# Optimization experiments

Hardware: AMD Instinct MI355X
Metric: run time of the kernel (lower is better)

## Reference

```python
import jax, jax.numpy as jnp
import numpy as np

B, S, HID = 1, 4096, 1024
NH, HD = 16, 64            # heads, per-head dim
BS = 256                    # block size
PB = 256                    # position buckets (= max_relative_positions)
EPS = 1e-7


def make_log_bucket_position(rel, num_buckets, max_position):
    sign = jnp.sign(rel)
    max_exact = num_buckets // 2
    in_exact = (rel < max_exact) & (rel > -max_exact)
    abs_pos = jnp.where(in_exact, max_exact - 1, jnp.abs(rel))
    x = jnp.log((max_position - 1) / max_exact)
    xx = jnp.log(abs_pos / max_exact) / x
    log_pos = jnp.ceil(xx * (max_exact - 1)) + max_exact
    return jnp.where(abs_pos <= max_exact, rel, (log_pos * sign).astype(jnp.int32)).astype(jnp.int32)


def split_into_blocks(x, block_size, axis):
    # [..., S, ...] -> [..., S//bs, bs, ...]; S assumed divisible by bs
    shp = x.shape
    new = shp[:axis] + (shp[axis] // block_size, block_size) + shp[axis + 1:]
    return x.reshape(new)


def concat_3_blocks(x, block_axis, seq_axis, pad_value=0):
    # pad one zero block on each side of the block axis, then concat
    # [prev, cur, next] along the within-block seq axis.
    pad = [(0, 0)] * x.ndim
    pad[block_axis] = (1, 1)
    xp = jnp.pad(x, pad, constant_values=pad_value)
    nb = x.shape[block_axis]
    slices = [jax.lax.dynamic_slice_in_dim(xp, i, nb, block_axis) for i in range(3)]
    return jnp.concatenate(slices, axis=seq_axis)


def layer_norm(x, scale, bias):
    mu = jnp.mean(x, axis=-1, keepdims=True)
    var = jnp.mean(jnp.square(x - mu), axis=-1, keepdims=True)
    return (x - mu) * jax.lax.rsqrt(var + EPS) * scale + bias


def setup_inputs() -> dict:
    key = jax.random.key(0)
    ks = jax.random.split(key, 8)
    d = {
        'hidden_states': jax.random.normal(ks[0], (B, S, HID), jnp.float32) * 0.02,
        'rel_pos_embeddings': jax.random.normal(ks[1], (S, HID), jnp.float32) * 0.02,
        'Wq': jax.random.normal(ks[2], (HID, HID), jnp.float32) * 0.01,
        'bq': jnp.zeros((HID,), jnp.float32),
        'Wk': jax.random.normal(ks[3], (HID, HID), jnp.float32) * 0.01,
        'bk': jnp.zeros((HID,), jnp.float32),
        'Wv': jax.random.normal(ks[4], (HID, HID), jnp.float32) * 0.01,
        'bv': jnp.zeros((HID,), jnp.float32),
        'Wo': jax.random.normal(ks[5], (HID, HID), jnp.float32) * 0.01,
        'bo': jnp.zeros((HID,), jnp.float32),
        'ln_scale': jnp.ones((HID,), jnp.float32),
        'ln_bias': jnp.zeros((HID,), jnp.float32),
    }
    return d


def reference(hidden_states, rel_pos_embeddings, Wq, bq, Wk, bk, Wv, bv, Wo, bo, ln_scale, ln_bias):
    b, s, hid = hidden_states.shape

    def heads(x):
        return x.reshape(x.shape[:-1] + (NH, HD))

    # content projections -> [B, nb, bs, h, d]
    q = split_into_blocks(heads(hidden_states @ Wq + bq), BS, axis=1)
    k = split_into_blocks(heads(hidden_states @ Wk + bk), BS, axis=1)
    v = split_into_blocks(heads(hidden_states @ Wv + bv), BS, axis=1)
    k3 = concat_3_blocks(k, block_axis=1, seq_axis=2)   # [B, nb, 3bs, h, d]
    v3 = concat_3_blocks(v, block_axis=1, seq_axis=2)

    c2c = jnp.einsum('bnqhd,bnkhd->bnhqk', q, k3)

    # position projections, stacked over batch (size-1 batch dim broadcasts in einsum)
    pos_q = split_into_blocks(heads(rel_pos_embeddings @ Wq + bq)[None], BS, axis=1)  # [1, nb, bs, h, d]
    pos_k = split_into_blocks(heads(rel_pos_embeddings @ Wk + bk)[None], BS, axis=1)
    pos_k3 = concat_3_blocks(pos_k, block_axis=1, seq_axis=2)                          # [1, nb, 3bs, h, d]

    rel = jnp.arange(BS, dtype=jnp.int32)[:, None] - jnp.arange(3 * BS, dtype=jnp.int32)[None, :]
    rel = make_log_bucket_position(rel, PB, PB)
    idx = jnp.clip(rel + PB, 0, 2 * PB - 1)            # [bs, 3bs]

    c2p = jnp.einsum('bnqhd,bnkhd->bnhqk', q, pos_k3)  # [B, nb, h, bs, 3bs]
    # faithful to the source: axis-less jnp.take gathers from the FLATTENED
    # score tensor -> [bs, 3bs] bias broadcast over (batch, block, head)
    c2p_bias = jnp.take(c2p, idx)

    p2c = jnp.einsum('bnqhd,bnkhd->bnhqk', pos_q, k3)
    p2c_bias = jnp.take(p2c, idx)

    scale = jnp.sqrt(jnp.asarray(HD * 3, hidden_states.dtype))
    attn = (c2c + c2p_bias + p2c_bias) / scale
    probs = jax.nn.softmax(attn, axis=-1)

    ctx = jnp.einsum('bnhqk,bnkhd->bnqhd', probs, v3)  # [B, nb, bs, h, d]
    ctx = ctx.reshape(b, s, hid)
    out = ctx @ Wo + bo
    return layer_norm(out + hidden_states, ln_scale, ln_bias)
```

## Files before the change

### kernel.cpp

```cpp
#include <hip/hip_runtime.h>
#include <stdint.h>

typedef unsigned short u16;
typedef __bf16 bf16_t;
typedef bf16_t v8bf __attribute__((ext_vector_type(8)));
typedef float v4f __attribute__((ext_vector_type(4)));

#define SEQ   4096
#define HIDN  1024
#define NHEAD 16
#define HDIM  64
#define BLK   256
#define NBLK  16

#define GLOAD_LDS16(g, l) __builtin_amdgcn_global_load_lds( \
  (const __attribute__((address_space(1))) unsigned*)(g), \
  (__attribute__((address_space(3))) unsigned*)(l), 16, 0, 0)

__device__ __forceinline__ u16 f2bf(float f){
  union { float f; unsigned u; } v; v.f = f;
  unsigned r = (v.u + 0x7fffu + ((v.u >> 16) & 1u)) >> 16;
  return (u16)r;
}
__device__ __forceinline__ float bf2f(u16 h){
  union { unsigned u; float f; } v; v.u = ((unsigned)h) << 16;
  return v.f;
}

__global__ __launch_bounds__(256) void k_prep(const float* __restrict__ hidden, u16* __restrict__ hb,
    const float* __restrict__ Wq, const float* __restrict__ Wk,
    const float* __restrict__ Wv, const float* __restrict__ Wo, u16* __restrict__ Wt,
    const float* __restrict__ bq, const float* __restrict__ bk, const float* __restrict__ bv,
    float* __restrict__ bcat,
    const float* __restrict__ rpe, float* __restrict__ posk, float* __restrict__ posq0)
{
  __shared__ float t[32][33];
  __shared__ float red[4][64];
  int b = blockIdx.x, tid = threadIdx.x;
  if (b < 4096){
    int w = b >> 10, tile = b & 1023;
    int k0 = (tile & 31) * 32, n0 = (tile >> 5) * 32;
    const float* W = (w == 0) ? Wq : (w == 1) ? Wk : (w == 2) ? Wv : Wo;
    u16* outp = Wt + (size_t)w * 1024 * 1024;
    int x = tid & 31, y = tid >> 5;
    #pragma unroll
    for (int yy = 0; yy < 32; yy += 8) t[y + yy][x] = W[(size_t)(k0 + y + yy) * 1024 + n0 + x];
    __syncthreads();
    #pragma unroll
    for (int yy = 0; yy < 32; yy += 8) outp[(size_t)(n0 + y + yy) * 1024 + k0 + x] = f2bf(t[x][y + yy]);
  } else if (b < 4608){
    int base = (b - 4096) * 8192;
    #pragma unroll
    for (int j = 0; j < 8; j++){
      int i = base + j * 1024 + tid * 4;
      float4 f = *(const float4*)&hidden[i];
      unsigned u0 = (unsigned)f2bf(f.x) | ((unsigned)f2bf(f.y) << 16);
      unsigned u1 = (unsigned)f2bf(f.z) | ((unsigned)f2bf(f.w) << 16);
      uint2 p; p.x = u0; p.y = u1;
      *(uint2*)&hb[i] = p;
    }
  } else if (b == 4608){
    #pragma unroll
    for (int j = 0; j < 12; j++){
      int i = j * 256 + tid;
      const float* src = i < 1024 ? bq : (i < 2048 ? bk : bv);
      bcat[i] = src[i & 1023];
    }
  } else {
    int pb = b - 4609;
    int d = tid & 63, part = tid >> 6;
    const float* W  = (pb < 256) ? Wk : Wq;
    const float* rv = (pb < 256) ? &rpe[(size_t)pb * 1024] : rpe;
    float s = 0.f;
    for (int k = part * 256; k < part * 256 + 256; k++) s += rv[k] * W[(size_t)k * 1024 + d];
    red[part][d] = s;
    __syncthreads();
    if (part == 0){
      s = red[0][d] + red[1][d] + red[2][d] + red[3][d];
      if (pb < 256) posk[pb * 64 + d] = s + bk[d];
      else          posq0[d] = s + bq[d];
    }
  }
}

__global__ __launch_bounds__(256) void k_gemm_qkv(const u16* __restrict__ A, const u16* __restrict__ Bt,
                                                  const float* __restrict__ bias,
                                                  u16* __restrict__ qk, u16* __restrict__ Vt)
{
  __shared__ alignas(16) u16 As[128 * 32];
  __shared__ alignas(16) u16 Bs[128 * 32];
  int tid = threadIdx.x, lane = tid & 63, wid = tid >> 6;
  int wr = wid >> 1, wc = wid & 1;
  int m0 = blockIdx.y * 128, n0 = blockIdx.x * 128;
  const int K = 1024;

  v4f acc[4][4];
  #pragma unroll
  for (int m = 0; m < 4; m++)
    #pragma unroll
    for (int n = 0; n < 4; n++) acc[m][n] = (v4f){0.f, 0.f, 0.f, 0.f};

  int r = lane & 15, g = lane >> 4;
  int ob0 = wid * 2048;

  for (int kt = 0; kt < K; kt += 32){
    #pragma unroll
    for (int t = 0; t < 2; ++t){
      int ob = ob0 + t * 1024;
      int o  = ob + lane * 16;
      int row = o >> 6, col = (o & 63) >> 1;
      GLOAD_LDS16(&A [(size_t)(m0 + row) * K + kt + col], As + (ob >> 1));
      GLOAD_LDS16(&Bt[(size_t)(n0 + row) * K + kt + col], Bs + (ob >> 1));
    }
    __syncthreads();
    v8bf a[4], bb[4];
    #pragma unroll
    for (int m = 0; m < 4; m++) a[m] = *(const v8bf*)&As[(wr * 64 + m * 16 + r) * 32 + g * 8];
    #pragma unroll
    for (int n = 0; n < 4; n++) bb[n] = *(const v8bf*)&Bs[(wc * 64 + n * 16 + r) * 32 + g * 8];
    #pragma unroll
    for (int m = 0; m < 4; m++)
      #pragma unroll
      for (int n = 0; n < 4; n++)
        acc[m][n] = __builtin_amdgcn_mfma_f32_16x16x32_bf16(a[m], bb[n], acc[m][n], 0, 0, 0);
    __syncthreads();
  }

  #pragma unroll
  for (int m = 0; m < 4; m++)
    #pragma unroll
    for (int n = 0; n < 4; n++){
      int col = n0 + wc * 64 + n * 16 + r;
      float bv = bias[col];
      #pragma unroll
      for (int i = 0; i < 4; i++){
        int row = m0 + wr * 64 + m * 16 + g * 4 + i;
        u16 h = f2bf(acc[m][n][i] + bv);
        if (col < 2048) qk[(size_t)row * 2048 + col] = h;
        else            Vt[(size_t)(col - 2048) * 4096 + row] = h;
      }
    }
}

__global__ __launch_bounds__(256) void k_gemm_out(const u16* __restrict__ A, const u16* __restrict__ Bt,
                                                  const float* __restrict__ bias,
                                                  const float* __restrict__ resid, float* __restrict__ Cout)
{
  __shared__ alignas(16) u16 As[128 * 32];
  __shared__ alignas(16) u16 Bs[128 * 32];
  int tid = threadIdx.x, lane = tid & 63, wid = tid >> 6;
  int wr = wid >> 1, wc = wid & 1;
  int m0 = blockIdx.y * 128, n0 = blockIdx.x * 128;
  const int K = 1024;

  v4f acc[4][4];
  #pragma unroll
  for (int m = 0; m < 4; m++)
    #pragma unroll
    for (int n = 0; n < 4; n++) acc[m][n] = (v4f){0.f, 0.f, 0.f, 0.f};

  int r = lane & 15, g = lane >> 4;
  int ob0 = wid * 2048;

  for (int kt = 0; kt < K; kt += 32){
    #pragma unroll
    for (int t = 0; t < 2; ++t){
      int ob = ob0 + t * 1024;
      int o  = ob + lane * 16;
      int row = o >> 6, col = (o & 63) >> 1;
      GLOAD_LDS16(&A [(size_t)(m0 + row) * K + kt + col], As + (ob >> 1));
      GLOAD_LDS16(&Bt[(size_t)(n0 + row) * K + kt + col], Bs + (ob >> 1));
    }
    __syncthreads();
    v8bf a[4], bb[4];
    #pragma unroll
    for (int m = 0; m < 4; m++) a[m] = *(const v8bf*)&As[(wr * 64 + m * 16 + r) * 32 + g * 8];
    #pragma unroll
    for (int n = 0; n < 4; n++) bb[n] = *(const v8bf*)&Bs[(wc * 64 + n * 16 + r) * 32 + g * 8];
    #pragma unroll
    for (int m = 0; m < 4; m++)
      #pragma unroll
      for (int n = 0; n < 4; n++)
        acc[m][n] = __builtin_amdgcn_mfma_f32_16x16x32_bf16(a[m], bb[n], acc[m][n], 0, 0, 0);
    __syncthreads();
  }

  #pragma unroll
  for (int m = 0; m < 4; m++)
    #pragma unroll
    for (int n = 0; n < 4; n++){
      int col = n0 + wc * 64 + n * 16 + r;
      float bv = bias[col];
      #pragma unroll
      for (int i = 0; i < 4; i++){
        int row = m0 + wr * 64 + m * 16 + g * 4 + i;
        Cout[(size_t)row * 1024 + col] = acc[m][n][i] + bv + resid[(size_t)row * 1024 + col];
      }
    }
}

__global__ __launch_bounds__(256) void k_bias(const u16* __restrict__ qk,
                                              const float* __restrict__ posk, const float* __restrict__ posq0,
                                              float* __restrict__ biasd)
{
  __shared__ float brow[512];
  int tid = threadIdx.x;
  brow[tid] = 0.f;
  {
    int u = tid;
    float c2p = 0.f, p2c = 0.f;
    for (int d = 0; d < 64; d++){
      c2p += bf2f(qk[d]) * posk[u * 64 + d];
      p2c += posq0[d] * bf2f(qk[(size_t)u * 2048 + 1024 + d]);
    }
    brow[256 + u] = c2p + p2c;
  }
  __syncthreads();
  #pragma unroll
  for (int j = 0; j < 4; j++){
    int t = tid + j * 256;
    int rel = t - 767;
    int bucket;
    bool in_exact = (rel < 128) && (rel > -128);
    int abs_pos = in_exact ? 127 : (rel < 0 ? -rel : rel);
    if (abs_pos <= 128) bucket = rel;
    else {
      float xx = logf((float)abs_pos * (1.0f / 128.0f)) / logf(255.0f / 128.0f);
      float lp = ceilf(xx * 127.0f) + 128.0f;
      int sgn = (rel > 0) ? 1 : ((rel < 0) ? -1 : 0);
      bucket = (int)lp * sgn;
    }
    int idx = bucket + 256;
    idx = idx < 0 ? 0 : (idx > 511 ? 511 : idx);
    biasd[t] = brow[idx];
  }
}

__global__ __launch_bounds__(256) void k_attn(const u16* __restrict__ qk, const u16* __restrict__ Vt,
                                              const float* __restrict__ biasd, u16* __restrict__ ctxg)
{
  __shared__ alignas(16) u16 Qs[32 * 72];
  __shared__ alignas(16) u16 KVs[128 * 72];
  __shared__ alignas(16) u16 Ss[32 * 776];
  __shared__ float invsum[32];
  __shared__ float bias_s[1024];

  int b = blockIdx.x;
  int qt = b & 7, h = (b >> 3) & 15, n = b >> 7;
  int tid = threadIdx.x, lane = tid & 63, wid = tid >> 6;
  int q0 = n * 256 + qt * 32;
  int qb0 = qt * 32;
  int g0 = (n - 1) * 256;
  const float inv_scale = 0.07216878364870323f;

  {
    int row = tid >> 3, seg = tid & 7;
    *(uint4*)&Qs[row * 72 + seg * 8] =
      *(const uint4*)&qk[(size_t)(q0 + row) * 2048 + h * 64 + seg * 8];
    *(float4*)&bias_s[tid * 4] = *(const float4*)&biasd[tid * 4];
  }
  __syncthreads();

  int r = lane & 15, g = lane >> 4;
  int qf = wid >> 1;
  int kh = wid & 1;
  int dh = wid & 1;

  for (int c = 0; c < 6; ++c){
    int cb = g0 + c * 128;
    bool oob = (cb < 0) || (cb >= SEQ);
    if (!oob){
      #pragma unroll
      for (int it = 0; it < 2; ++it){
        int row = it * 64 + (tid >> 2), seg = tid & 3;
        const u16* src = &qk[(size_t)(cb + row) * 2048 + 1024 + h * 64 + seg * 16];
        *(uint4*)&KVs[row * 72 + seg * 16]     = *(const uint4*)&src[0];
        *(uint4*)&KVs[row * 72 + seg * 16 + 8] = *(const uint4*)&src[8];
      }
    }
    __syncthreads();
    v4f sacc[4];
    #pragma unroll
    for (int nn = 0; nn < 4; nn++) sacc[nn] = (v4f){0.f,0.f,0.f,0.f};
    if (!oob){
      #pragma unroll
      for (int ks = 0; ks < 2; ++ks){
        v8bf a = *(const v8bf*)&Qs[(qf * 16 + r) * 72 + ks * 32 + g * 8];
        #pragma unroll
        for (int nn = 0; nn < 4; nn++){
          v8bf bb = *(const v8bf*)&KVs[(kh * 64 + nn * 16 + r) * 72 + ks * 32 + g * 8];
          sacc[nn] = __builtin_amdgcn_mfma_f32_16x16x32_bf16(a, bb, sacc[nn], 0, 0, 0);
        }
      }
    }
    #pragma unroll
    for (int nn = 0; nn < 4; nn++){
      int kcol = c * 128 + kh * 64 + nn * 16 + r;
      int scol = kcol ^ (g << 4);
      #pragma unroll
      for (int i = 0; i < 4; i++){
        int qrow = qf * 16 + g * 4 + i;
        float sc = (sacc[nn][i] + bias_s[qb0 + qrow - kcol + 767]) * inv_scale;
        Ss[qrow * 776 + scol] = f2bf(sc);
      }
    }
    __syncthreads();
  }

  {
    int row = tid >> 3, sub = tid & 7;
    u16* srow = &Ss[row * 776 + sub * 96];
    float mx = -3.0e38f;
    #pragma unroll
    for (int ii = 0; ii < 12; ii++){
      uint4 pk = *(const uint4*)&srow[ii * 8];
      const unsigned* w = (const unsigned*)&pk;
      #pragma unroll
      for (int j = 0; j < 4; j++){
        mx = fmaxf(mx, bf2f((u16)(w[j] & 0xffff)));
        mx = fmaxf(mx, bf2f((u16)(w[j] >> 16)));
      }
    }
    mx = fmaxf(mx, __shfl_xor(mx, 1));
    mx = fmaxf(mx, __shfl_xor(mx, 2));
    mx = fmaxf(mx, __shfl_xor(mx, 4));
    float sm = 0.f;
    #pragma unroll
    for (int ii = 0; ii < 12; ii++){
      uint4 pk = *(const uint4*)&srow[ii * 8];
      unsigned* w = (unsigned*)&pk;
      #pragma unroll
      for (int j = 0; j < 4; j++){
        float e0 = __expf(bf2f((u16)(w[j] & 0xffff)) - mx);
        float e1 = __expf(bf2f((u16)(w[j] >> 16)) - mx);
        sm += e0 + e1;
        w[j] = (unsigned)f2bf(e0) | ((unsigned)f2bf(e1) << 16);
      }
      *(uint4*)&srow[ii * 8] = pk;
    }
    sm += __shfl_xor(sm, 1);
    sm += __shfl_xor(sm, 2);
    sm += __shfl_xor(sm, 4);
    if (sub == 0) invsum[row] = 1.0f / sm;
  }
  __syncthreads();

  v4f pacc[2];
  pacc[0] = (v4f){0.f,0.f,0.f,0.f};
  pacc[1] = (v4f){0.f,0.f,0.f,0.f};
  int swr = ((r >> 2) & 3) << 4;
  for (int c = 0; c < 6; ++c){
    int cb = g0 + c * 128;
    bool oob = (cb < 0) || (cb >= SEQ);
    if (!oob){
      int d = tid >> 2, seg = tid & 3;
      const u16* src = &Vt[(size_t)(h * 64 + d) * 4096 + cb];
      #pragma unroll
      for (int ii = 0; ii < 4; ii++)
        *(uint4*)&KVs[d * 136 + (ii * 4 + seg) * 8] = *(const uint4*)&src[(ii * 4 + seg) * 8];
    }
    __syncthreads();
    if (!oob){
      #pragma unroll
      for (int ks = 0; ks < 4; ++ks){
        v8bf a = *(const v8bf*)&Ss[(qf * 16 + r) * 776 + ((c * 128 + ks * 32 + g * 8) ^ swr)];
        #pragma unroll
        for (int nn = 0; nn < 2; nn++){
          v8bf bb = *(const v8bf*)&KVs[(dh * 32 + nn * 16 + r) * 136 + ks * 32 + g * 8];
          pacc[nn] = __builtin_amdgcn_mfma_f32_16x16x32_bf16(a, bb, pacc[nn], 0, 0, 0);
        }
      }
    }
    __syncthreads();
  }
  #pragma unroll
  for (int nn = 0; nn < 2; nn++){
    int d = dh * 32 + nn * 16 + r;
    #pragma unroll
    for (int i = 0; i < 4; i++){
      int qrow = qf * 16 + g * 4 + i;
      float val = pacc[nn][i] * invsum[qrow];
      ctxg[(size_t)(q0 + qrow) * 1024 + h * 64 + d] = f2bf(val);
    }
  }
}

__global__ __launch_bounds__(256) void k_ln(float* __restrict__ out,
                                            const float* __restrict__ gamma, const float* __restrict__ beta)
{
  __shared__ float red[8];
  int row = blockIdx.x, tid = threadIdx.x;
  int lane = tid & 63, wid = tid >> 6;
  size_t base = (size_t)row * 1024 + tid * 4;
  float4 xv = *(const float4*)&out[base];
  float v0 = xv.x, v1 = xv.y, v2 = xv.z, v3 = xv.w;
  float s = v0 + v1 + v2 + v3;
  float q = v0 * v0 + v1 * v1 + v2 * v2 + v3 * v3;
  #pragma unroll
  for (int o = 32; o; o >>= 1){ s += __shfl_down(s, o); q += __shfl_down(q, o); }
  if (lane == 0){ red[wid] = s; red[4 + wid] = q; }
  __syncthreads();
  float ts = red[0] + red[1] + red[2] + red[3];
  float tq = red[4] + red[5] + red[6] + red[7];
  float mu = ts * (1.0f / 1024.0f);
  float var = tq * (1.0f / 1024.0f) - mu * mu;
  float rstd = rsqrtf(var + 1e-7f);
  int c = tid * 4;
  out[base + 0] = (v0 - mu) * rstd * gamma[c + 0] + beta[c + 0];
  out[base + 1] = (v1 - mu) * rstd * gamma[c + 1] + beta[c + 1];
  out[base + 2] = (v2 - mu) * rstd * gamma[c + 2] + beta[c + 2];
  out[base + 3] = (v3 - mu) * rstd * gamma[c + 3] + beta[c + 3];
}

extern "C" void kernel_launch(void* const* d_in, const int* in_sizes, int n_in,
                              void* d_out, int out_size, void* d_ws, size_t ws_size,
                              hipStream_t stream)
{
  const float* hidden = (const float*)d_in[0];
  const float* rpe    = (const float*)d_in[1];
  const float* Wq = (const float*)d_in[2];
  const float* bq = (const float*)d_in[3];
  const float* Wk = (const float*)d_in[4];
  const float* bk = (const float*)d_in[5];
  const float* Wv = (const float*)d_in[6];
  const float* bv = (const float*)d_in[7];
  const float* Wo = (const float*)d_in[8];
  const float* bo = (const float*)d_in[9];
  const float* lns = (const float*)d_in[10];
  const float* lnb = (const float*)d_in[11];
  float* out = (float*)d_out;

  char* ws = (char*)d_ws;
  size_t off = 0;
  auto alloc = [&](size_t bytes){ void* p = ws + off; off += (bytes + 255) & ~(size_t)255; return p; };
  u16* hb      = (u16*)alloc((size_t)SEQ * HIDN * 2);
  u16* Wt      = (u16*)alloc((size_t)4 * HIDN * HIDN * 2);
  u16* qk      = (u16*)alloc((size_t)SEQ * 2048 * 2);
  u16* Vt      = (u16*)alloc((size_t)HIDN * SEQ * 2);
  u16* ctxb    = (u16*)alloc((size_t)SEQ * HIDN * 2);
  float* bcat  = (float*)alloc(3072 * 4);
  float* poskf = (float*)alloc(256 * 64 * 4);
  float* posq0 = (float*)alloc(64 * 4);
  float* biasd = (float*)alloc(1024 * 4);
  (void)ws_size; (void)in_sizes; (void)n_in; (void)out_size;

  k_prep<<<4866, 256, 0, stream>>>(hidden, hb, Wq, Wk, Wv, Wo, Wt,
                                   bq, bk, bv, bcat, rpe, poskf, posq0);

  k_gemm_qkv<<<dim3(24, 32), 256, 0, stream>>>(hb, Wt, bcat, qk, Vt);

  k_bias<<<1, 256, 0, stream>>>(qk, poskf, posq0, biasd);

  k_attn<<<NBLK * NHEAD * 8, 256, 0, stream>>>(qk, Vt, biasd, ctxb);

  k_gemm_out<<<dim3(8, 32), 256, 0, stream>>>(ctxb, Wt + (size_t)3 * HIDN * HIDN, bo, hidden, out);

  k_ln<<<SEQ, 256, 0, stream>>>(out, lns, lnb);
}
```

Before: 172.7 us.

## Halve attention query tile, use direct global-to-LDS loads with XOR swizzle

The attention kernel now handles 16 query rows per block instead of 32, which doubles the grid to 4096 blocks. Q, K and V tiles are loaded with global_load_lds straight into XOR-swizzled LDS layouts, replacing register-staged copies into padded rows. The row max is now tracked in registers during the score pass and reduced across waves, so the softmax makes one pass over the scores instead of two. The smaller tile raises parallelism and cuts LDS use, but each block reloads K and V for fewer queries, which doubles K/V traffic.

```diff
diff --git a/kernel.cpp b/kernel.cpp
--- a/kernel.cpp
+++ b/kernel.cpp
@@ -239,148 +239,150 @@
 __global__ __launch_bounds__(256) void k_attn(const u16* __restrict__ qk, const u16* __restrict__ Vt,
                                               const float* __restrict__ biasd, u16* __restrict__ ctxg)
 {
-  __shared__ alignas(16) u16 Qs[32 * 72];
-  __shared__ alignas(16) u16 KVs[128 * 72];
-  __shared__ alignas(16) u16 Ss[32 * 776];
-  __shared__ float invsum[32];
+  __shared__ alignas(16) u16 Qs[16 * 64];
+  __shared__ alignas(16) u16 KVs[8192];
+  __shared__ alignas(16) u16 Ss[16 * 776];
   __shared__ float bias_s[1024];
+  __shared__ float wmax[64];
+  __shared__ float invsum[16];
 
   int b = blockIdx.x;
-  int qt = b & 7, h = (b >> 3) & 15, n = b >> 7;
-  int tid = threadIdx.x, lane = tid & 63, wid = tid >> 6;
-  int q0 = n * 256 + qt * 32;
-  int qb0 = qt * 32;
+  int qt = b & 15, h = (b >> 4) & 15, n = b >> 8;
+  int tid = threadIdx.x, lane = tid & 63, w = tid >> 6;
+  int q0 = n * 256 + qt * 16;
+  int qb0 = qt * 16;
   int g0 = (n - 1) * 256;
   const float inv_scale = 0.07216878364870323f;
 
-  {
-    int row = tid >> 3, seg = tid & 7;
-    *(uint4*)&Qs[row * 72 + seg * 8] =
-      *(const uint4*)&qk[(size_t)(q0 + row) * 2048 + h * 64 + seg * 8];
-    *(float4*)&bias_s[tid * 4] = *(const float4*)&biasd[tid * 4];
-  }
-  __syncthreads();
-
   int r = lane & 15, g = lane >> 4;
-  int qf = wid >> 1;
-  int kh = wid & 1;
-  int dh = wid & 1;
+
+  if (w < 2){
+    int o = w * 1024 + lane * 16;
+    int row = o >> 7, p = (o >> 4) & 7;
+    GLOAD_LDS16(&qk[(size_t)(q0 + row) * 2048 + h * 64 + ((p ^ (row & 7)) * 8)],
+                ((u16*)Qs) + w * 512);
+  }
+  *(float4*)&bias_s[tid * 4] = *(const float4*)&biasd[tid * 4];
+
+  float m4[4];
+  #pragma unroll
+  for (int i = 0; i < 4; i++) m4[i] = -3.0e38f;
 
   for (int c = 0; c < 6; ++c){
     int cb = g0 + c * 128;
     bool oob = (cb < 0) || (cb >= SEQ);
     if (!oob){
       #pragma unroll
-      for (int it = 0; it < 2; ++it){
-        int row = it * 64 + (tid >> 2), seg = tid & 3;
-        const u16* src = &qk[(size_t)(cb + row) * 2048 + 1024 + h * 64 + seg * 16];
-        *(uint4*)&KVs[row * 72 + seg * 16]     = *(const uint4*)&src[0];
-        *(uint4*)&KVs[row * 72 + seg * 16 + 8] = *(const uint4*)&src[8];
-      }
-    }
-    __syncthreads();
-    v4f sacc[4];
-    #pragma unroll
-    for (int nn = 0; nn < 4; nn++) sacc[nn] = (v4f){0.f,0.f,0.f,0.f};
+      for (int t = 0; t < 4; ++t){
+        int o = (w * 4 + t) * 1024 + lane * 16;
+        int row = o >> 7, p = (o >> 4) & 7;
+        GLOAD_LDS16(&qk[(size_t)(cb + row) * 2048 + 1024 + h * 64 + ((p ^ (row & 7)) * 8)],
+                    ((u16*)KVs) + (w * 4 + t) * 512);
+      }
+    }
+    __syncthreads();
+    v4f sacc[2];
+    sacc[0] = (v4f){0.f,0.f,0.f,0.f};
+    sacc[1] = (v4f){0.f,0.f,0.f,0.f};
     if (!oob){
       #pragma unroll
       for (int ks = 0; ks < 2; ++ks){
-        v8bf a = *(const v8bf*)&Qs[(qf * 16 + r) * 72 + ks * 32 + g * 8];
+        v8bf a = *(const v8bf*)&Qs[r * 64 + ((4 * ks + g) ^ (r & 7)) * 8];
         #pragma unroll
-        for (int nn = 0; nn < 4; nn++){
-          v8bf bb = *(const v8bf*)&KVs[(kh * 64 + nn * 16 + r) * 72 + ks * 32 + g * 8];
+        for (int nn = 0; nn < 2; nn++){
+          int kr = w * 32 + nn * 16 + r;
+          v8bf bb = *(const v8bf*)&KVs[kr * 64 + ((4 * ks + g) ^ (kr & 7)) * 8];
           sacc[nn] = __builtin_amdgcn_mfma_f32_16x16x32_bf16(a, bb, sacc[nn], 0, 0, 0);
         }
       }
     }
     #pragma unroll
-    for (int nn = 0; nn < 4; nn++){
-      int kcol = c * 128 + kh * 64 + nn * 16 + r;
+    for (int nn = 0; nn < 2; nn++){
+      int kcol = c * 128 + w * 32 + nn * 16 + r;
       int scol = kcol ^ (g << 4);
       #pragma unroll
       for (int i = 0; i < 4; i++){
-        int qrow = qf * 16 + g * 4 + i;
+        int qrow = g * 4 + i;
         float sc = (sacc[nn][i] + bias_s[qb0 + qrow - kcol + 767]) * inv_scale;
+        m4[i] = fmaxf(m4[i], sc);
         Ss[qrow * 776 + scol] = f2bf(sc);
       }
     }
     __syncthreads();
   }
 
+  #pragma unroll
+  for (int i = 0; i < 4; i++){
+    m4[i] = fmaxf(m4[i], __shfl_xor(m4[i], 1));
+    m4[i] = fmaxf(m4[i], __shfl_xor(m4[i], 2));
+    m4[i] = fmaxf(m4[i], __shfl_xor(m4[i], 4));
+    m4[i] = fmaxf(m4[i], __shfl_xor(m4[i], 8));
+  }
+  if (r == 0){
+    #pragma unroll
+    for (int i = 0; i < 4; i++) wmax[w * 16 + g * 4 + i] = m4[i];
+  }
+  __syncthreads();
+
   {
-    int row = tid >> 3, sub = tid & 7;
-    u16* srow = &Ss[row * 776 + sub * 96];
-    float mx = -3.0e38f;
-    #pragma unroll
-    for (int ii = 0; ii < 12; ii++){
+    int row = tid >> 4, sub = tid & 15;
+    float mx = fmaxf(fmaxf(wmax[row], wmax[16 + row]), fmaxf(wmax[32 + row], wmax[48 + row]));
+    u16* srow = &Ss[row * 776 + sub * 48];
+    float sm = 0.f;
+    #pragma unroll
+    for (int ii = 0; ii < 6; ii++){
       uint4 pk = *(const uint4*)&srow[ii * 8];
-      const unsigned* w = (const unsigned*)&pk;
+      unsigned* wd = (unsigned*)&pk;
       #pragma unroll
       for (int j = 0; j < 4; j++){
-        mx = fmaxf(mx, bf2f((u16)(w[j] & 0xffff)));
-        mx = fmaxf(mx, bf2f((u16)(w[j] >> 16)));
-      }
-    }
-    mx = fmaxf(mx, __shfl_xor(mx, 1));
-    mx = fmaxf(mx, __shfl_xor(mx, 2));
-    mx = fmaxf(mx, __shfl_xor(mx, 4));
-    float sm = 0.f;
-    #pragma unroll
-    for (int ii = 0; ii < 12; ii++){
-      uint4 pk = *(const uint4*)&srow[ii * 8];
-      unsigned* w = (unsigned*)&pk;
-      #pragma unroll
-      for (int j = 0; j < 4; j++){
-        float e0 = __expf(bf2f((u16)(w[j] & 0xffff)) - mx);
-        float e1 = __expf(bf2f((u16)(w[j] >> 16)) - mx);
+        float e0 = __expf(bf2f((u16)(wd[j] & 0xffff)) - mx);
+        float e1 = __expf(bf2f((u16)(wd[j] >> 16)) - mx);
         sm += e0 + e1;
-        w[j] = (unsigned)f2bf(e0) | ((unsigned)f2bf(e1) << 16);
+        wd[j] = (unsigned)f2bf(e0) | ((unsigned)f2bf(e1) << 16);
       }
       *(uint4*)&srow[ii * 8] = pk;
     }
     sm += __shfl_xor(sm, 1);
     sm += __shfl_xor(sm, 2);
     sm += __shfl_xor(sm, 4);
+    sm += __shfl_xor(sm, 8);
     if (sub == 0) invsum[row] = 1.0f / sm;
   }
   __syncthreads();
 
-  v4f pacc[2];
-  pacc[0] = (v4f){0.f,0.f,0.f,0.f};
-  pacc[1] = (v4f){0.f,0.f,0.f,0.f};
-  int swr = ((r >> 2) & 3) << 4;
+  v4f pacc = (v4f){0.f,0.f,0.f,0.f};
+  int key = (r >> 2) & 3;
   for (int c = 0; c < 6; ++c){
     int cb = g0 + c * 128;
     bool oob = (cb < 0) || (cb >= SEQ);
     if (!oob){
-      int d = tid >> 2, seg = tid & 3;
-      const u16* src = &Vt[(size_t)(h * 64 + d) * 4096 + cb];
-      #pragma unroll
-      for (int ii = 0; ii < 4; ii++)
-        *(uint4*)&KVs[d * 136 + (ii * 4 + seg) * 8] = *(const uint4*)&src[(ii * 4 + seg) * 8];
+      #pragma unroll
+      for (int t = 0; t < 4; ++t){
+        int o = (w * 4 + t) * 1024 + lane * 16;
+        int d = o >> 8, p = (o >> 4) & 15;
+        GLOAD_LDS16(&Vt[(size_t)(h * 64 + d) * 4096 + cb + ((p ^ (d & 7)) * 8)],
+                    ((u16*)KVs) + (w * 4 + t) * 512);
+      }
     }
     __syncthreads();
     if (!oob){
+      int d = w * 16 + r;
       #pragma unroll
       for (int ks = 0; ks < 4; ++ks){
-        v8bf a = *(const v8bf*)&Ss[(qf * 16 + r) * 776 + ((c * 128 + ks * 32 + g * 8) ^ swr)];
-        #pragma unroll
-        for (int nn = 0; nn < 2; nn++){
-          v8bf bb = *(const v8bf*)&KVs[(dh * 32 + nn * 16 + r) * 136 + ks * 32 + g * 8];
-          pacc[nn] = __builtin_amdgcn_mfma_f32_16x16x32_bf16(a, bb, pacc[nn], 0, 0, 0);
-        }
-      }
-    }
-    __syncthreads();
-  }
-  #pragma unroll
-  for (int nn = 0; nn < 2; nn++){
-    int d = dh * 32 + nn * 16 + r;
+        int col = (c * 128 + ks * 32 + g * 8) ^ (key << 4);
+        v8bf a  = *(const v8bf*)&Ss[r * 776 + col];
+        v8bf bb = *(const v8bf*)&KVs[d * 128 + ((4 * ks + g) ^ (r & 7)) * 8];
+        pacc = __builtin_amdgcn_mfma_f32_16x16x32_bf16(a, bb, pacc, 0, 0, 0);
+      }
+    }
+    __syncthreads();
+  }
+  {
+    int d = w * 16 + r;
     #pragma unroll
     for (int i = 0; i < 4; i++){
-      int qrow = qf * 16 + g * 4 + i;
-      float val = pacc[nn][i] * invsum[qrow];
-      ctxg[(size_t)(q0 + qrow) * 1024 + h * 64 + d] = f2bf(val);
+      int qrow = g * 4 + i;
+      ctxg[(size_t)(q0 + qrow) * 1024 + h * 64 + d] = f2bf(pacc[i] * invsum[qrow]);
     }
   }
 }
@@ -451,7 +453,7 @@
 
   k_bias<<<1, 256, 0, stream>>>(qk, poskf, posq0, biasd);
 
-  k_attn<<<NBLK * NHEAD * 8, 256, 0, stream>>>(qk, Vt, biasd, ctxb);
+  k_attn<<<NBLK * NHEAD * 16, 256, 0, stream>>>(qk, Vt, biasd, ctxb);
 
   k_gemm_out<<<dim3(8, 32), 256, 0, stream>>>(ctxb, Wt + (size_t)3 * HIDN * HIDN, bo, hidden, out);
 
```

Result: no change. 174.4 us (+0.9%).
